# Kernel tuning notes

Measured on AMD Instinct MI355X. Metric: run time of the kernel, lower is better.

The kernel has to match this reference:

```python
import jax, jax.numpy as jnp
import numpy as np

B, N, D = 65536, 512, 512


def setup_inputs() -> dict:
    key = jax.random.key(0)
    k1, k2 = jax.random.split(key)
    # sample_orthonormal_vectors(n, d): QR of a (d, n) gaussian matrix, rows are codes
    rm = np.asarray(jax.random.normal(k1, (D, N), dtype=jnp.float32))
    Q, _ = np.linalg.qr(rm, mode='complete')  # Q: (d, d)
    codebook_vectors = jnp.asarray(Q.T[:, :N].T, dtype=jnp.float32)  # (n, d), w = 1.0
    batch_z = jax.random.normal(k2, (B, D), dtype=jnp.float32)
    return {"batch_z": batch_z, "codebook_vectors": codebook_vectors}


def reference(batch_z, codebook_vectors):
    """Faithful jax version of Codebook.closest_z.

    torch code materializes a (B, n, d) broadcast diff then norms over dim=2.
    Same math via the expanded squared-distance identity (no (B,n,d) tensor):
      ||z - c||^2 = ||z||^2 + ||c||^2 - 2 z.c
    """
    n, d = codebook_vectors.shape
    z = batch_z.reshape(-1, d)  # (B, d)
    z_sq = jnp.sum(z * z, axis=1, keepdims=True)                # (B, 1)
    c_sq = jnp.sum(codebook_vectors * codebook_vectors, axis=1)  # (n,)
    sq_dist = z_sq + c_sq[None, :] - 2.0 * (z @ codebook_vectors.T)  # (B, n)
    distances = jnp.sqrt(jnp.maximum(sq_dist, 0.0))
    indices = jnp.argmin(distances, axis=1)                      # (B,)
    one_hot = jax.nn.one_hot(indices, n, dtype=jnp.float32)      # eye(n)[indices]
    return one_hot, indices
```

## Files before the change

kernel.cpp:

```cpp
#include <hip/hip_runtime.h>
#include <math.h>

#define BQ 65536
#define NC 512
#define DD 512
#define BM 128
#define BN 256
#define BK 32
#define MARGIN 3e-3f
#define FINF 3.402823466e38f

typedef short bf16x8 __attribute__((ext_vector_type(8)));
typedef float f32x4 __attribute__((ext_vector_type(4)));

#define AHI 0
#define ALO 2560
#define BHI 5120
#define BLO 10240
#define STRIDE 20

__device__ __forceinline__ unsigned int cvt_pk_bf16(float a, float b) {
    unsigned int r;
    asm("v_cvt_pk_bf16_f32 %0, %1, %2" : "=v"(r) : "v"(a), "v"(b));
    return r;
}

__device__ __forceinline__ void split4(float4 v, uint2* hi, uint2* lo) {
    unsigned int h0 = cvt_pk_bf16(v.x, v.y);
    unsigned int h1 = cvt_pk_bf16(v.z, v.w);
    float hx = __uint_as_float(h0 << 16);
    float hy = __uint_as_float(h0 & 0xFFFF0000u);
    float hz = __uint_as_float(h1 << 16);
    float hw = __uint_as_float(h1 & 0xFFFF0000u);
    *hi = make_uint2(h0, h1);
    *lo = make_uint2(cvt_pk_bf16(v.x - hx, v.y - hy),
                     cvt_pk_bf16(v.z - hz, v.w - hw));
}

__device__ __forceinline__ float pw128_sq(const float* __restrict__ p) {
    float r[8];
    #pragma unroll
    for (int j = 0; j < 8; ++j) r[j] = 0.0f;
    #pragma unroll
    for (int q = 0; q < 32; ++q) {
        float4 v = *(const float4*)(p + q * 4);
        const int e = (q & 1) << 2;
        r[e + 0] = __fadd_rn(r[e + 0], __fmul_rn(v.x, v.x));
        r[e + 1] = __fadd_rn(r[e + 1], __fmul_rn(v.y, v.y));
        r[e + 2] = __fadd_rn(r[e + 2], __fmul_rn(v.z, v.z));
        r[e + 3] = __fadd_rn(r[e + 3], __fmul_rn(v.w, v.w));
    }
    return __fadd_rn(__fadd_rn(__fadd_rn(r[0], r[1]), __fadd_rn(r[2], r[3])),
                     __fadd_rn(__fadd_rn(r[4], r[5]), __fadd_rn(r[6], r[7])));
}

__global__ __launch_bounds__(256, 2) void codebook_kernel(
    const float* __restrict__ Z, const float* __restrict__ Cb,
    float* __restrict__ out, int* __restrict__ wslist, int cap) {

    __shared__ __align__(16) unsigned int stage[15360];
    __shared__ float csq[NC];
    __shared__ float red_b1[2][BM];
    __shared__ float red_b2[2][BM];
    __shared__ int   red_i1[2][BM];
    __shared__ int   bif[BM];

    const int tid = threadIdx.x;
    const int m0 = blockIdx.x * BM;
    const int l = tid & 63, wid = tid >> 6;
    const int wr0 = (wid >> 1) * 64;
    const int wc0 = (wid & 1) * 128;
    const int g = l >> 4, c = l & 15;

    #pragma unroll
    for (int cc = 0; cc < 2; ++cc) {
        const int code = tid + cc * 256;
        const float* p = Cb + (size_t)code * DD;
        float b0 = pw128_sq(p), b1 = pw128_sq(p + 128);
        float b2 = pw128_sq(p + 256), b3 = pw128_sq(p + 384);
        csq[code] = __fadd_rn(__fadd_rn(b0, b1), __fadd_rn(b2, b3));
    }

    float rb1 = FINF, rb2 = FINF; int ri1 = 0;

    float4 va[4], vb[8];
    #pragma unroll
    for (int p = 0; p < 4; ++p) {
        int q = tid + p * 256;
        va[p] = *(const float4*)(Z + (size_t)(m0 + (q >> 3)) * DD + (q & 7) * 4);
    }
    #pragma unroll
    for (int p = 0; p < 8; ++p) {
        int q = tid + p * 256;
        vb[p] = *(const float4*)(Cb + (size_t)(q >> 3) * DD + (q & 7) * 4);
    }

    f32x4 acc[4][8];

    for (int step = 0; step < 32; ++step) {
        const int kt = (step & 15) * BK;
        const int n0 = (step >> 4) * BN;
        if ((step & 15) == 0) {
            #pragma unroll
            for (int i = 0; i < 4; ++i)
                #pragma unroll
                for (int j = 0; j < 8; ++j) acc[i][j] = (f32x4)0.0f;
        }
        __syncthreads();
        #pragma unroll
        for (int p = 0; p < 4; ++p) {
            int q = tid + p * 256;
            int r = q >> 3, k2 = (q & 7) * 2;
            uint2 h, lo;
            split4(va[p], &h, &lo);
            *(uint2*)&stage[AHI + r * STRIDE + k2] = h;
            *(uint2*)&stage[ALO + r * STRIDE + k2] = lo;
        }
        #pragma unroll
        for (int p = 0; p < 8; ++p) {
            int q = tid + p * 256;
            int r = q >> 3, k2 = (q & 7) * 2;
            uint2 h, lo;
            split4(vb[p], &h, &lo);
            *(uint2*)&stage[BHI + r * STRIDE + k2] = h;
            *(uint2*)&stage[BLO + r * STRIDE + k2] = lo;
        }
        __syncthreads();
        if (step < 31) {
            const int kt2 = ((step + 1) & 15) * BK;
            const int n02 = ((step + 1) >> 4) * BN;
            #pragma unroll
            for (int p = 0; p < 4; ++p) {
                int q = tid + p * 256;
                va[p] = *(const float4*)(Z + (size_t)(m0 + (q >> 3)) * DD + kt2 + (q & 7) * 4);
            }
            #pragma unroll
            for (int p = 0; p < 8; ++p) {
                int q = tid + p * 256;
                vb[p] = *(const float4*)(Cb + (size_t)(n02 + (q >> 3)) * DD + kt2 + (q & 7) * 4);
            }
        }
        bf16x8 ah[4], al[4];
        #pragma unroll
        for (int i = 0; i < 4; ++i) {
            int R = wr0 + i * 16 + c;
            ah[i] = *(bf16x8*)&stage[AHI + R * STRIDE + g * 4];
            al[i] = *(bf16x8*)&stage[ALO + R * STRIDE + g * 4];
        }
        #pragma unroll
        for (int j = 0; j < 8; ++j) {
            int C = wc0 + j * 16 + c;
            bf16x8 bh = *(bf16x8*)&stage[BHI + C * STRIDE + g * 4];
            bf16x8 bl = *(bf16x8*)&stage[BLO + C * STRIDE + g * 4];
            #pragma unroll
            for (int i = 0; i < 4; ++i) {
                acc[i][j] = __builtin_amdgcn_mfma_f32_16x16x32_bf16(ah[i], bh, acc[i][j], 0, 0, 0);
                acc[i][j] = __builtin_amdgcn_mfma_f32_16x16x32_bf16(ah[i], bl, acc[i][j], 0, 0, 0);
                acc[i][j] = __builtin_amdgcn_mfma_f32_16x16x32_bf16(al[i], bh, acc[i][j], 0, 0, 0);
            }
        }
        (void)kt;

        if ((step & 15) == 15) {
            #pragma unroll
            for (int i = 0; i < 4; ++i) {
                #pragma unroll
                for (int r = 0; r < 4; ++r) {
                    float b1 = FINF, b2 = FINF; int i1 = 0;
                    #pragma unroll
                    for (int j = 0; j < 8; ++j) {
                        int code = n0 + wc0 + j * 16 + c;
                        float m = fmaf(-2.0f, acc[i][j][r], csq[code]);
                        if (m < b1) { b2 = b1; b1 = m; i1 = code; }
                        else b2 = fminf(b2, m);
                    }
                    #pragma unroll
                    for (int s = 1; s < 16; s <<= 1) {
                        float ob1 = __shfl_xor(b1, s);
                        float ob2 = __shfl_xor(b2, s);
                        int oi1 = __shfl_xor(i1, s);
                        if (ob1 < b1 || (ob1 == b1 && oi1 < i1)) {
                            b2 = fminf(b1, ob2); b1 = ob1; i1 = oi1;
                        } else {
                            b2 = fminf(b2, ob1);
                        }
                    }
                    if (c == 0) {
                        int row = wr0 + i * 16 + g * 4 + r;
                        red_b1[wid & 1][row] = b1;
                        red_b2[wid & 1][row] = b2;
                        red_i1[wid & 1][row] = i1;
                    }
                }
            }
            __syncthreads();
            if (tid < BM) {
                #pragma unroll
                for (int h = 0; h < 2; ++h) {
                    float nb1 = red_b1[h][tid], nb2 = red_b2[h][tid];
                    int ni = red_i1[h][tid];
                    if (nb1 < rb1) { rb2 = fminf(rb1, nb2); rb1 = nb1; ri1 = ni; }
                    else rb2 = fminf(rb2, nb1);
                }
            }
        }
    }

    if (tid < BM) {
        bif[tid] = ri1;
        out[(size_t)BQ * NC + m0 + tid] = (float)ri1;
        if (rb2 - rb1 < MARGIN) {
            int slot = atomicAdd(wslist, 1);
            if (slot < cap) wslist[1 + slot] = m0 + tid;
        }
    }
    __syncthreads();

    #pragma unroll 4
    for (int t = 0; t < 64; ++t) {
        int f4i = tid + t * 256;
        int r = f4i >> 7, c4 = f4i & 127;
        int tgt = bif[r];
        int base = c4 * 4;
        float4 v;
        v.x = (tgt == base + 0) ? 1.0f : 0.0f;
        v.y = (tgt == base + 1) ? 1.0f : 0.0f;
        v.z = (tgt == base + 2) ? 1.0f : 0.0f;
        v.w = (tgt == base + 3) ? 1.0f : 0.0f;
        *(float4*)(out + (size_t)(m0 + r) * NC + (size_t)base) = v;
    }
}

__global__ __launch_bounds__(256) void fixup_kernel(
    const float* __restrict__ Z, const float* __restrict__ Cb,
    float* __restrict__ out, const int* __restrict__ wslist, int cap) {

    __shared__ float zrow[DD];
    __shared__ double md[256];
    __shared__ int mi[256];
    const int tid = threadIdx.x;
    int count = wslist[0];
    if (count > cap) count = cap;

    for (int e = blockIdx.x; e < count; e += gridDim.x) {
        const int row = wslist[1 + e];
        zrow[tid] = Z[(size_t)row * DD + tid];
        zrow[tid + 256] = Z[(size_t)row * DD + 256 + tid];
        __syncthreads();

        double bb = 1e300; int bidx = 0;
        #pragma unroll
        for (int cc = 0; cc < 2; ++cc) {
            const int code = tid * 2 + cc;
            const float* cp = Cb + (size_t)code * DD;
            double dot = 0.0, cs = 0.0;
            for (int k = 0; k < DD; k += 4) {
                float4 c4 = *(const float4*)(cp + k);
                double a0 = (double)zrow[k + 0], c0 = (double)c4.x;
                double a1 = (double)zrow[k + 1], c1 = (double)c4.y;
                double a2 = (double)zrow[k + 2], c2 = (double)c4.z;
                double a3 = (double)zrow[k + 3], c3 = (double)c4.w;
                dot = fma(a0, c0, dot); cs = fma(c0, c0, cs);
                dot = fma(a1, c1, dot); cs = fma(c1, c1, cs);
                dot = fma(a2, c2, dot); cs = fma(c2, c2, cs);
                dot = fma(a3, c3, dot); cs = fma(c3, c3, cs);
            }
            double m = cs - 2.0 * dot;
            if (m < bb || (m == bb && code < bidx)) { bb = m; bidx = code; }
        }
        md[tid] = bb; mi[tid] = bidx;
        __syncthreads();
        for (int s = 128; s > 0; s >>= 1) {
            if (tid < s) {
                if (md[tid + s] < md[tid] ||
                    (md[tid + s] == md[tid] && mi[tid + s] < mi[tid])) {
                    md[tid] = md[tid + s]; mi[tid] = mi[tid + s];
                }
            }
            __syncthreads();
        }
        const int imin = mi[0];
        out[(size_t)row * NC + tid] = (tid == imin) ? 1.0f : 0.0f;
        out[(size_t)row * NC + 256 + tid] = (tid + 256 == imin) ? 1.0f : 0.0f;
        if (tid == 0) out[(size_t)BQ * NC + row] = (float)imin;
        __syncthreads();
    }
}

extern "C" void kernel_launch(void* const* d_in, const int* in_sizes, int n_in,
                              void* d_out, int out_size, void* d_ws, size_t ws_size,
                              hipStream_t stream) {
    const float* Z = (const float*)d_in[0];
    const float* Cb = (const float*)d_in[1];
    float* out = (float*)d_out;
    int* wslist = (int*)d_ws;
    int cap = (int)(ws_size / 4) - 1;
    if (cap > BQ) cap = BQ;
    hipMemsetAsync(d_ws, 0, 4, stream);
    codebook_kernel<<<dim3(BQ / BM), dim3(256), 0, stream>>>(Z, Cb, out, wslist, cap);
    fixup_kernel<<<dim3(512), dim3(256), 0, stream>>>(Z, Cb, out, wslist, cap);
}
```

Baseline: 264.5 us.

## Stream fp32 tiles directly into LDS and split to bf16 at fragment load

Replaces the register-prefetch path, which loaded float4s, split them into bf16 hi/lo and stored both halves to LDS, with global_load_lds DMA of raw fp32 tiles into an XOR-swizzled LDS layout. The hi/lo split now happens after each fragment read from LDS. The reduction scratch arrays are aliased onto the stage buffer, behind an extra barrier, to cut shared memory use, and the minimum-occupancy launch bound is dropped. The cost is that the split is recomputed per wave for every fragment use, and the global loads are no longer overlapped with compute because there is a single buffer with no prefetch.

```diff
diff --git a/kernel.cpp b/kernel.cpp
--- a/kernel.cpp
+++ b/kernel.cpp
@@ -13,11 +13,11 @@
 typedef short bf16x8 __attribute__((ext_vector_type(8)));
 typedef float f32x4 __attribute__((ext_vector_type(4)));
 
-#define AHI 0
-#define ALO 2560
-#define BHI 5120
-#define BLO 10240
-#define STRIDE 20
+__device__ __forceinline__ void load_lds16(const float* g, unsigned int* l) {
+    __builtin_amdgcn_global_load_lds(
+        (const __attribute__((address_space(1))) unsigned int*)(const void*)g,
+        (__attribute__((address_space(3))) unsigned int*)(void*)l, 16, 0, 0);
+}
 
 __device__ __forceinline__ unsigned int cvt_pk_bf16(float a, float b) {
     unsigned int r;
@@ -25,16 +25,23 @@
     return r;
 }
 
-__device__ __forceinline__ void split4(float4 v, uint2* hi, uint2* lo) {
-    unsigned int h0 = cvt_pk_bf16(v.x, v.y);
-    unsigned int h1 = cvt_pk_bf16(v.z, v.w);
-    float hx = __uint_as_float(h0 << 16);
-    float hy = __uint_as_float(h0 & 0xFFFF0000u);
-    float hz = __uint_as_float(h1 << 16);
-    float hw = __uint_as_float(h1 & 0xFFFF0000u);
-    *hi = make_uint2(h0, h1);
-    *lo = make_uint2(cvt_pk_bf16(v.x - hx, v.y - hy),
-                     cvt_pk_bf16(v.z - hz, v.w - hw));
+__device__ __forceinline__ void cvt8(float4 f0, float4 f1,
+                                     bf16x8* hi, bf16x8* lo) {
+    unsigned int h01 = cvt_pk_bf16(f0.x, f0.y);
+    unsigned int h23 = cvt_pk_bf16(f0.z, f0.w);
+    unsigned int h45 = cvt_pk_bf16(f1.x, f1.y);
+    unsigned int h67 = cvt_pk_bf16(f1.z, f1.w);
+    float a0 = __uint_as_float(h01 << 16), a1 = __uint_as_float(h01 & 0xFFFF0000u);
+    float a2 = __uint_as_float(h23 << 16), a3 = __uint_as_float(h23 & 0xFFFF0000u);
+    float a4 = __uint_as_float(h45 << 16), a5 = __uint_as_float(h45 & 0xFFFF0000u);
+    float a6 = __uint_as_float(h67 << 16), a7 = __uint_as_float(h67 & 0xFFFF0000u);
+    union { bf16x8 v; unsigned int u[4]; } H, L;
+    H.u[0] = h01; H.u[1] = h23; H.u[2] = h45; H.u[3] = h67;
+    L.u[0] = cvt_pk_bf16(f0.x - a0, f0.y - a1);
+    L.u[1] = cvt_pk_bf16(f0.z - a2, f0.w - a3);
+    L.u[2] = cvt_pk_bf16(f1.x - a4, f1.y - a5);
+    L.u[3] = cvt_pk_bf16(f1.z - a6, f1.w - a7);
+    *hi = H.v; *lo = L.v;
 }
 
 __device__ __forceinline__ float pw128_sq(const float* __restrict__ p) {
@@ -54,16 +61,13 @@
                      __fadd_rn(__fadd_rn(r[4], r[5]), __fadd_rn(r[6], r[7])));
 }
 
-__global__ __launch_bounds__(256, 2) void codebook_kernel(
+__global__ __launch_bounds__(256) void codebook_kernel(
     const float* __restrict__ Z, const float* __restrict__ Cb,
     float* __restrict__ out, int* __restrict__ wslist, int cap) {
 
-    __shared__ __align__(16) unsigned int stage[15360];
+    __shared__ __align__(16) unsigned int stage[12288];
     __shared__ float csq[NC];
-    __shared__ float red_b1[2][BM];
-    __shared__ float red_b2[2][BM];
-    __shared__ int   red_i1[2][BM];
-    __shared__ int   bif[BM];
+    __shared__ int bif[BM];
 
     const int tid = threadIdx.x;
     const int m0 = blockIdx.x * BM;
@@ -82,19 +86,6 @@
     }
 
     float rb1 = FINF, rb2 = FINF; int ri1 = 0;
-
-    float4 va[4], vb[8];
-    #pragma unroll
-    for (int p = 0; p < 4; ++p) {
-        int q = tid + p * 256;
-        va[p] = *(const float4*)(Z + (size_t)(m0 + (q >> 3)) * DD + (q & 7) * 4);
-    }
-    #pragma unroll
-    for (int p = 0; p < 8; ++p) {
-        int q = tid + p * 256;
-        vb[p] = *(const float4*)(Cb + (size_t)(q >> 3) * DD + (q & 7) * 4);
-    }
-
     f32x4 acc[4][8];
 
     for (int step = 0; step < 32; ++step) {
@@ -108,50 +99,36 @@
         }
         __syncthreads();
         #pragma unroll
-        for (int p = 0; p < 4; ++p) {
-            int q = tid + p * 256;
-            int r = q >> 3, k2 = (q & 7) * 2;
-            uint2 h, lo;
-            split4(va[p], &h, &lo);
-            *(uint2*)&stage[AHI + r * STRIDE + k2] = h;
-            *(uint2*)&stage[ALO + r * STRIDE + k2] = lo;
-        }
-        #pragma unroll
-        for (int p = 0; p < 8; ++p) {
-            int q = tid + p * 256;
-            int r = q >> 3, k2 = (q & 7) * 2;
-            uint2 h, lo;
-            split4(vb[p], &h, &lo);
-            *(uint2*)&stage[BHI + r * STRIDE + k2] = h;
-            *(uint2*)&stage[BLO + r * STRIDE + k2] = lo;
-        }
-        __syncthreads();
-        if (step < 31) {
-            const int kt2 = ((step + 1) & 15) * BK;
-            const int n02 = ((step + 1) >> 4) * BN;
-            #pragma unroll
-            for (int p = 0; p < 4; ++p) {
-                int q = tid + p * 256;
-                va[p] = *(const float4*)(Z + (size_t)(m0 + (q >> 3)) * DD + kt2 + (q & 7) * 4);
-            }
-            #pragma unroll
-            for (int p = 0; p < 8; ++p) {
-                int q = tid + p * 256;
-                vb[p] = *(const float4*)(Cb + (size_t)(n02 + (q >> 3)) * DD + kt2 + (q & 7) * 4);
-            }
-        }
+        for (int i = 0; i < 4; ++i) {
+            int n = tid + i * 256;
+            int R = n >> 3, u = (n & 7) ^ (R & 7);
+            load_lds16(Z + (size_t)(m0 + R) * DD + kt + u * 4, &stage[n * 4]);
+        }
+        #pragma unroll
+        for (int i = 0; i < 8; ++i) {
+            int n = tid + i * 256;
+            int C = n >> 3, u = (n & 7) ^ (C & 7);
+            load_lds16(Cb + (size_t)(n0 + C) * DD + kt + u * 4, &stage[4096 + n * 4]);
+        }
+        __syncthreads();
+
         bf16x8 ah[4], al[4];
         #pragma unroll
         for (int i = 0; i < 4; ++i) {
             int R = wr0 + i * 16 + c;
-            ah[i] = *(bf16x8*)&stage[AHI + R * STRIDE + g * 4];
-            al[i] = *(bf16x8*)&stage[ALO + R * STRIDE + g * 4];
+            const unsigned int* ar = &stage[R * 32];
+            float4 f0 = *(const float4*)&ar[((2 * g) ^ (R & 7)) * 4];
+            float4 f1 = *(const float4*)&ar[((2 * g + 1) ^ (R & 7)) * 4];
+            cvt8(f0, f1, &ah[i], &al[i]);
         }
         #pragma unroll
         for (int j = 0; j < 8; ++j) {
             int C = wc0 + j * 16 + c;
-            bf16x8 bh = *(bf16x8*)&stage[BHI + C * STRIDE + g * 4];
-            bf16x8 bl = *(bf16x8*)&stage[BLO + C * STRIDE + g * 4];
+            const unsigned int* br = &stage[4096 + C * 32];
+            float4 f0 = *(const float4*)&br[((2 * g) ^ (C & 7)) * 4];
+            float4 f1 = *(const float4*)&br[((2 * g + 1) ^ (C & 7)) * 4];
+            bf16x8 bh, bl;
+            cvt8(f0, f1, &bh, &bl);
             #pragma unroll
             for (int i = 0; i < 4; ++i) {
                 acc[i][j] = __builtin_amdgcn_mfma_f32_16x16x32_bf16(ah[i], bh, acc[i][j], 0, 0, 0);
@@ -159,9 +136,12 @@
                 acc[i][j] = __builtin_amdgcn_mfma_f32_16x16x32_bf16(al[i], bh, acc[i][j], 0, 0, 0);
             }
         }
-        (void)kt;
 
         if ((step & 15) == 15) {
+            __syncthreads();
+            float* red_b1 = (float*)stage;
+            int*   red_i1 = (int*)(stage + 256);
+            float* red_b2 = (float*)(stage + 512);
             #pragma unroll
             for (int i = 0; i < 4; ++i) {
                 #pragma unroll
@@ -187,9 +167,9 @@
                     }
                     if (c == 0) {
                         int row = wr0 + i * 16 + g * 4 + r;
-                        red_b1[wid & 1][row] = b1;
-                        red_b2[wid & 1][row] = b2;
-                        red_i1[wid & 1][row] = i1;
+                        red_b1[(wid & 1) * BM + row] = b1;
+                        red_b2[(wid & 1) * BM + row] = b2;
+                        red_i1[(wid & 1) * BM + row] = i1;
                     }
                 }
             }
@@ -197,8 +177,8 @@
             if (tid < BM) {
                 #pragma unroll
                 for (int h = 0; h < 2; ++h) {
-                    float nb1 = red_b1[h][tid], nb2 = red_b2[h][tid];
-                    int ni = red_i1[h][tid];
+                    float nb1 = red_b1[h * BM + tid], nb2 = red_b2[h * BM + tid];
+                    int ni = red_i1[h * BM + tid];
                     if (nb1 < rb1) { rb2 = fminf(rb1, nb2); rb1 = nb1; ri1 = ni; }
                     else rb2 = fminf(rb2, nb1);
                 }
```

Result: slower. 357.8 us (+35.3%).

## Load codebook fragments directly into registers, bypassing LDS staging

Applied to the files above, without the earlier changes.

Each wave now loads its own codebook operand fragments straight from global memory into registers in MFMA layout and splits them into bf16 hi/lo there, removing the B-side LDS writes and reads. The codebook loads for the next step are issued inside the MFMA loop so they overlap with compute. This shrinks LDS use and LDS traffic. In exchange, codebook data is loaded redundantly by the two waves that share columns, and the 64 float registers of prefetch add register pressure that may reduce occupancy under the launch bounds.

```diff
diff --git a/kernel.cpp b/kernel.cpp
--- a/kernel.cpp
+++ b/kernel.cpp
@@ -15,8 +15,6 @@
 
 #define AHI 0
 #define ALO 2560
-#define BHI 5120
-#define BLO 10240
 #define STRIDE 20
 
 __device__ __forceinline__ unsigned int cvt_pk_bf16(float a, float b) {
@@ -37,6 +35,25 @@
                      cvt_pk_bf16(v.z - hz, v.w - hw));
 }
 
+__device__ __forceinline__ void cvt8(float4 f0, float4 f1,
+                                     bf16x8* hi, bf16x8* lo) {
+    unsigned int h01 = cvt_pk_bf16(f0.x, f0.y);
+    unsigned int h23 = cvt_pk_bf16(f0.z, f0.w);
+    unsigned int h45 = cvt_pk_bf16(f1.x, f1.y);
+    unsigned int h67 = cvt_pk_bf16(f1.z, f1.w);
+    float a0 = __uint_as_float(h01 << 16), a1 = __uint_as_float(h01 & 0xFFFF0000u);
+    float a2 = __uint_as_float(h23 << 16), a3 = __uint_as_float(h23 & 0xFFFF0000u);
+    float a4 = __uint_as_float(h45 << 16), a5 = __uint_as_float(h45 & 0xFFFF0000u);
+    float a6 = __uint_as_float(h67 << 16), a7 = __uint_as_float(h67 & 0xFFFF0000u);
+    union { bf16x8 v; unsigned int u[4]; } H, L;
+    H.u[0] = h01; H.u[1] = h23; H.u[2] = h45; H.u[3] = h67;
+    L.u[0] = cvt_pk_bf16(f0.x - a0, f0.y - a1);
+    L.u[1] = cvt_pk_bf16(f0.z - a2, f0.w - a3);
+    L.u[2] = cvt_pk_bf16(f1.x - a4, f1.y - a5);
+    L.u[3] = cvt_pk_bf16(f1.z - a6, f1.w - a7);
+    *hi = H.v; *lo = L.v;
+}
+
 __device__ __forceinline__ float pw128_sq(const float* __restrict__ p) {
     float r[8];
     #pragma unroll
@@ -58,7 +75,7 @@
     const float* __restrict__ Z, const float* __restrict__ Cb,
     float* __restrict__ out, int* __restrict__ wslist, int cap) {
 
-    __shared__ __align__(16) unsigned int stage[15360];
+    __shared__ __align__(16) unsigned int stage[5120];
     __shared__ float csq[NC];
     __shared__ float red_b1[2][BM];
     __shared__ float red_b2[2][BM];
@@ -83,23 +100,28 @@
 
     float rb1 = FINF, rb2 = FINF; int ri1 = 0;
 
-    float4 va[4], vb[8];
+    float4 va[4];
     #pragma unroll
     for (int p = 0; p < 4; ++p) {
         int q = tid + p * 256;
         va[p] = *(const float4*)(Z + (size_t)(m0 + (q >> 3)) * DD + (q & 7) * 4);
     }
-    #pragma unroll
-    for (int p = 0; p < 8; ++p) {
-        int q = tid + p * 256;
-        vb[p] = *(const float4*)(Cb + (size_t)(q >> 3) * DD + (q & 7) * 4);
+    float4 vb[16];
+    #pragma unroll
+    for (int j = 0; j < 8; ++j) {
+        int C = wc0 + j * 16 + c;
+        vb[2 * j]     = *(const float4*)(Cb + (size_t)C * DD + g * 8);
+        vb[2 * j + 1] = *(const float4*)(Cb + (size_t)C * DD + g * 8 + 4);
     }
 
     f32x4 acc[4][8];
 
     for (int step = 0; step < 32; ++step) {
-        const int kt = (step & 15) * BK;
         const int n0 = (step >> 4) * BN;
+        const int nstep = (step < 31) ? step + 1 : 31;
+        const int ktn = (nstep & 15) * BK;
+        const int n0n = (nstep >> 4) * BN;
+
         if ((step & 15) == 0) {
             #pragma unroll
             for (int i = 0; i < 4; ++i)
@@ -116,28 +138,12 @@
             *(uint2*)&stage[AHI + r * STRIDE + k2] = h;
             *(uint2*)&stage[ALO + r * STRIDE + k2] = lo;
         }
-        #pragma unroll
-        for (int p = 0; p < 8; ++p) {
-            int q = tid + p * 256;
-            int r = q >> 3, k2 = (q & 7) * 2;
-            uint2 h, lo;
-            split4(vb[p], &h, &lo);
-            *(uint2*)&stage[BHI + r * STRIDE + k2] = h;
-            *(uint2*)&stage[BLO + r * STRIDE + k2] = lo;
-        }
         __syncthreads();
         if (step < 31) {
-            const int kt2 = ((step + 1) & 15) * BK;
-            const int n02 = ((step + 1) >> 4) * BN;
             #pragma unroll
             for (int p = 0; p < 4; ++p) {
                 int q = tid + p * 256;
-                va[p] = *(const float4*)(Z + (size_t)(m0 + (q >> 3)) * DD + kt2 + (q & 7) * 4);
-            }
-            #pragma unroll
-            for (int p = 0; p < 8; ++p) {
-                int q = tid + p * 256;
-                vb[p] = *(const float4*)(Cb + (size_t)(n02 + (q >> 3)) * DD + kt2 + (q & 7) * 4);
+                va[p] = *(const float4*)(Z + (size_t)(m0 + (q >> 3)) * DD + ktn + (q & 7) * 4);
             }
         }
         bf16x8 ah[4], al[4];
@@ -149,9 +155,13 @@
         }
         #pragma unroll
         for (int j = 0; j < 8; ++j) {
-            int C = wc0 + j * 16 + c;
-            bf16x8 bh = *(bf16x8*)&stage[BHI + C * STRIDE + g * 4];
-            bf16x8 bl = *(bf16x8*)&stage[BLO + C * STRIDE + g * 4];
+            bf16x8 bh, bl;
+            cvt8(vb[2 * j], vb[2 * j + 1], &bh, &bl);
+            {
+                int C = n0n + wc0 + j * 16 + c;
+                vb[2 * j]     = *(const float4*)(Cb + (size_t)C * DD + ktn + g * 8);
+                vb[2 * j + 1] = *(const float4*)(Cb + (size_t)C * DD + ktn + g * 8 + 4);
+            }
             #pragma unroll
             for (int i = 0; i < 4; ++i) {
                 acc[i][j] = __builtin_amdgcn_mfma_f32_16x16x32_bf16(ah[i], bh, acc[i][j], 0, 0, 0);
@@ -159,7 +169,6 @@
                 acc[i][j] = __builtin_amdgcn_mfma_f32_16x16x32_bf16(al[i], bh, acc[i][j], 0, 0, 0);
             }
         }
-        (void)kt;
 
         if ((step & 15) == 15) {
             #pragma unroll
```

Result: slower. 378.4 us (+43.1%).
